# Kernel tuning notes

Measured on AMD Instinct MI355X. Metric: run time of the kernel, lower is better.

Reference implementation:

```python
import jax, jax.numpy as jnp
import numpy as np

N = 500_000          # number of particles
D = 6                # phase-space dimension
N_BINS = 128         # bins per axis
SQRT2 = 1.4142135623730951
BANDWIDTH = 1.0      # kernel width relative to bin width (module default)


def setup_inputs() -> dict:
    key = jax.random.key(0)
    x = jax.random.normal(key, (N, D), dtype=jnp.float32)
    edges = jnp.linspace(-3.0, 3.0, N_BINS + 1, dtype=jnp.float32)
    return {"x": x, "bin_edges_x": edges, "bin_edges_y": edges}


def _cdf_weights(u, edges, bw):
    """Per-point Gaussian mass in each bin via CDF (erf) differences.

    u: (n,), edges: (m+1,) -> weights (n, m); row sums <= 1.
    """
    z = jax.scipy.special.erf((edges[None, :] - u[:, None]) / (bw * SQRT2))  # (n, m+1)
    return 0.5 * (z[:, 1:] - z[:, :-1])  # (n, m)


def reference(x, bin_edges_x, bin_edges_y):
    dx = bin_edges_x[1] - bin_edges_x[0]
    dy = bin_edges_y[1] - bin_edges_y[0]
    bw_x = BANDWIDTH * dx
    bw_y = BANDWIDTH * dy
    # axis = (0, 1): project onto first two phase-space coordinates
    wx = _cdf_weights(x[:, 0], bin_edges_x, bw_x)  # (n, bx)
    wy = _cdf_weights(x[:, 1], bin_edges_y, bw_y)  # (n, by)
    hist = jnp.einsum('ni,nj->ij', wx, wy)         # (bx, by)
    # normalize to a probability density over the grid
    hist = hist / (hist.sum() * dx * dy)
    return hist
```

## Files before the change

### kernel.cpp

```cpp
#include <hip/hip_runtime.h>
#include <math.h>


#define NBINS   128
#define NB2     (NBINS * NBINS)
#define LDH     129
#define THREADS 1024
#define NBLOCKS 256
#define QSCALE  320.0f

static __device__ __forceinline__ unsigned short f2bf(float f) {
    unsigned int b = __float_as_uint(f);
    b += 0x7fff + ((b >> 16) & 1);
    return (unsigned short)(b >> 16);
}
static __device__ __forceinline__ float bf2f(unsigned short u) {
    return __uint_as_float((unsigned int)u << 16);
}

static __device__ __forceinline__ float erf_fast(float x) {
    const float ax = fabsf(x);
    const float t  = __builtin_amdgcn_rcpf(fmaf(0.3275911f, ax, 1.0f));
    const float e  = __expf(-x * x);
    float p = fmaf(1.061405429f, t, -1.453152027f);
    p = fmaf(p, t, 1.421413741f);
    p = fmaf(p, t, -0.284496736f);
    p = fmaf(p, t, 0.254829592f);
    p = p * t;
    return copysignf(fmaf(-p, e, 1.0f), x);
}

static __device__ __forceinline__ void axis_q(
    float u, float e0, float inv, int& b0, int q[8])
{
    const float cc = 0.7071067811865476f;
    const float spos = (u - e0) * inv;
    int b = (int)floorf(spos + 0.5f) - 4;
    b0 = b < 0 ? 0 : (b > NBINS - 8 ? NBINS - 8 : b);
    const float t0 = ((float)b0 - spos) * cc;
    float z[9];
    #pragma unroll
    for (int k = 0; k < 9; ++k) z[k] = erf_fast(t0 + (float)k * cc);
    #pragma unroll
    for (int k = 0; k < 8; ++k)
        q[k] = (int)rintf(0.5f * (z[k + 1] - z[k]) * QSCALE);
}

__global__ __launch_bounds__(THREADS, 4) void hist_sparse_kernel(
    const float* __restrict__ x,
    const float* __restrict__ edges_x,
    const float* __restrict__ edges_y,
    unsigned short* __restrict__ partials,
    float* __restrict__ btot,
    int n)
{
    __shared__ int lh[NBINS * LDH];
    __shared__ int xw[16];

    const int tid  = threadIdx.x;
    const int lane = tid & 63;
    const int wv   = tid >> 6;

    for (int i = tid; i < NBINS * LDH; i += THREADS) lh[i] = 0;

    const float e0x = edges_x[0];
    const float dxw = edges_x[1] - e0x;
    const float e0y = edges_y[0];
    const float dyw = edges_y[1] - e0y;
    const float ivx = 1.0f / dxw;
    const float ivy = 1.0f / dyw;
    __syncthreads();

    int bsum = 0;
    const int stride = gridDim.x * THREADS;
    for (int p = blockIdx.x * THREADS + tid; p < n; p += stride) {
        const float2 u = *(const float2*)(x + (size_t)p * 6);
        int bx0, by0, qx[8], qy[8];
        axis_q(u.x, e0x, ivx, bx0, qx);
        axis_q(u.y, e0y, ivy, by0, qy);

        int sx = 0, sy = 0;
        #pragma unroll
        for (int k = 0; k < 8; ++k) { sx += qx[k]; sy += qy[k]; }
        bsum += sx * sy;

        int* const base = lh + bx0 * LDH + by0;
        #pragma unroll
        for (int i = 0; i < 8; ++i) {
            const int qi = qx[i];
            #pragma unroll
            for (int j = 0; j < 8; ++j)
                atomicAdd(base + i * LDH + j, qi * qy[j]);
        }
    }
    __syncthreads();

    {
        const float qs = 1.0f / (QSCALE * QSCALE);
        unsigned short* my = partials + (size_t)blockIdx.x * NB2;
        #pragma unroll
        for (int v = 0; v < 4; ++v) {
            const int e = tid * 16 + v * 4;
            const int r = e >> 7;
            const int c = e & 127;
            const int* row = lh + r * LDH + c;
            ushort4 o;
            o.x = f2bf((float)row[0] * qs);
            o.y = f2bf((float)row[1] * qs);
            o.z = f2bf((float)row[2] * qs);
            o.w = f2bf((float)row[3] * qs);
            *(ushort4*)(my + e) = o;
        }
    }

    #pragma unroll
    for (int off = 32; off > 0; off >>= 1) bsum += __shfl_down(bsum, off, 64);
    if (lane == 0) xw[wv] = bsum;
    __syncthreads();
    if (tid == 0) {
        const float qs = 1.0f / (QSCALE * QSCALE);
        int s = 0;
        #pragma unroll
        for (int k = 0; k < 16; ++k) s += xw[k];
        btot[blockIdx.x] = (float)s * qs;
    }
}

__global__ void reduce_kernel(const unsigned short* __restrict__ partials,
                              const float* __restrict__ btot,
                              const float* __restrict__ edges_x,
                              const float* __restrict__ edges_y,
                              float* __restrict__ out)
{
    __shared__ float4 red[16][16];
    __shared__ float ws[4];
    __shared__ float stot;

    const int t = threadIdx.x;
    const int bin4 = t & 15;
    const int pg = t >> 4;
    const int binBase = blockIdx.x * 64;

    float tl = btot[t];
    #pragma unroll
    for (int off = 32; off > 0; off >>= 1) tl += __shfl_down(tl, off, 64);
    if ((t & 63) == 0) ws[t >> 6] = tl;

    const unsigned short* p =
        partials + (size_t)(pg * 16) * NB2 + binBase + bin4 * 4;
    float4 s = {0.f, 0.f, 0.f, 0.f};
    #pragma unroll 8
    for (int k = 0; k < 16; ++k) {
        const ushort4 v = *(const ushort4*)(p + (size_t)k * NB2);
        s.x += bf2f(v.x); s.y += bf2f(v.y); s.z += bf2f(v.z); s.w += bf2f(v.w);
    }
    red[pg][bin4] = s;
    __syncthreads();

    if (t == 0) {
        const float dxw = edges_x[1] - edges_x[0];
        const float dyw = edges_y[1] - edges_y[0];
        stot = 1.0f / ((ws[0] + ws[1] + ws[2] + ws[3]) * dxw * dyw);
    }
    __syncthreads();

    if (t < 16) {
        float4 a = red[0][t];
        #pragma unroll
        for (int g = 1; g < 16; ++g) {
            const float4 b = red[g][t];
            a.x += b.x; a.y += b.y; a.z += b.z; a.w += b.w;
        }
        a.x *= stot; a.y *= stot; a.z *= stot; a.w *= stot;
        *(float4*)(out + binBase + t * 4) = a;
    }
}

extern "C" void kernel_launch(void* const* d_in, const int* in_sizes, int n_in,
                              void* d_out, int out_size, void* d_ws, size_t ws_size,
                              hipStream_t stream)
{
    const float* x  = (const float*)d_in[0];
    const float* ex = (const float*)d_in[1];
    const float* ey = (const float*)d_in[2];
    float* out = (float*)d_out;
    const int n = in_sizes[0] / 6;

    unsigned short* partials = (unsigned short*)d_ws;
    float* btot = (float*)((char*)d_ws + (size_t)NBLOCKS * NB2 * 2);

    hist_sparse_kernel<<<NBLOCKS, THREADS, 0, stream>>>(x, ex, ey, partials, btot, n);
    reduce_kernel<<<NB2 / 64, 256, 0, stream>>>(partials, btot, ex, ey, out);
}
```

Measured before the change: 76.39 us.

## Replace per-point erf evaluation with shared LUT and skip zero-weight atomics

Each block precomputes a 1024-entry shared-memory table of packed 8-bit quantized bin weights indexed by the fractional sub-bin offset. Per-particle erf evaluations become a table lookup plus byte unpacking. The 8-bin window is now centered on the particle instead of clamped at the edges, with explicit bounds checks. Atomic adds are skipped for zero products and wave-uniformly zero rows, which cuts LDS atomic traffic. The trade-off is quantization of the sub-bin position, which adds approximation error, plus extra branching.

```diff
diff --git a/kernel.cpp b/kernel.cpp
--- a/kernel.cpp
+++ b/kernel.cpp
@@ -30,22 +30,6 @@
     return copysignf(fmaf(-p, e, 1.0f), x);
 }
 
-static __device__ __forceinline__ void axis_q(
-    float u, float e0, float inv, int& b0, int q[8])
-{
-    const float cc = 0.7071067811865476f;
-    const float spos = (u - e0) * inv;
-    int b = (int)floorf(spos + 0.5f) - 4;
-    b0 = b < 0 ? 0 : (b > NBINS - 8 ? NBINS - 8 : b);
-    const float t0 = ((float)b0 - spos) * cc;
-    float z[9];
-    #pragma unroll
-    for (int k = 0; k < 9; ++k) z[k] = erf_fast(t0 + (float)k * cc);
-    #pragma unroll
-    for (int k = 0; k < 8; ++k)
-        q[k] = (int)rintf(0.5f * (z[k + 1] - z[k]) * QSCALE);
-}
-
 __global__ __launch_bounds__(THREADS, 4) void hist_sparse_kernel(
     const float* __restrict__ x,
     const float* __restrict__ edges_x,
@@ -55,12 +39,32 @@
     int n)
 {
     __shared__ int lh[NBINS * LDH];
+    __shared__ int2 lut[1024];
     __shared__ int xw[16];
 
     const int tid  = threadIdx.x;
     const int lane = tid & 63;
     const int wv   = tid >> 6;
 
+    {
+        const float cc = 0.7071067811865476f;
+        const float d = ((float)tid + 0.5f) * (1.0f / 1024.0f) - 0.5f;
+        float z[9];
+        #pragma unroll
+        for (int k = 0; k < 9; ++k)
+            z[k] = erf_fast(((float)k - 4.0f - d) * cc);
+        unsigned int lo = 0, hi = 0;
+        #pragma unroll
+        for (int k = 0; k < 4; ++k) {
+            const unsigned int qa =
+                (unsigned int)(int)rintf(0.5f * (z[k + 1] - z[k]) * QSCALE);
+            const unsigned int qb =
+                (unsigned int)(int)rintf(0.5f * (z[k + 5] - z[k + 4]) * QSCALE);
+            lo |= qa << (8 * k);
+            hi |= qb << (8 * k);
+        }
+        lut[tid] = make_int2((int)lo, (int)hi);
+    }
     for (int i = tid; i < NBINS * LDH; i += THREADS) lh[i] = 0;
 
     const float e0x = edges_x[0];
@@ -75,22 +79,52 @@
     const int stride = gridDim.x * THREADS;
     for (int p = blockIdx.x * THREADS + tid; p < n; p += stride) {
         const float2 u = *(const float2*)(x + (size_t)p * 6);
-        int bx0, by0, qx[8], qy[8];
-        axis_q(u.x, e0x, ivx, bx0, qx);
-        axis_q(u.y, e0y, ivy, by0, qy);
-
-        int sx = 0, sy = 0;
-        #pragma unroll
-        for (int k = 0; k < 8; ++k) { sx += qx[k]; sy += qy[k]; }
-        bsum += sx * sy;
-
-        int* const base = lh + bx0 * LDH + by0;
+
+        const float sposx = (u.x - e0x) * ivx;
+        const float rx = floorf(sposx + 0.5f);
+        const int b0x = (int)rx - 4;
+        int tix = (int)((sposx - rx + 0.5f) * 1024.0f);
+        tix = tix < 0 ? 0 : (tix > 1023 ? 1023 : tix);
+        const int2 wxp = lut[tix];
+
+        const float sposy = (u.y - e0y) * ivy;
+        const float ry = floorf(sposy + 0.5f);
+        const int b0y = (int)ry - 4;
+        int tiy = (int)((sposy - ry + 0.5f) * 1024.0f);
+        tiy = tiy < 0 ? 0 : (tiy > 1023 ? 1023 : tiy);
+        const int2 wyp = lut[tiy];
+
+        int qx[8], qy[8];
+        #pragma unroll
+        for (int k = 0; k < 4; ++k) {
+            qx[k]     = ((unsigned int)wxp.x >> (8 * k)) & 0xFF;
+            qx[k + 4] = ((unsigned int)wxp.y >> (8 * k)) & 0xFF;
+            qy[k]     = ((unsigned int)wyp.x >> (8 * k)) & 0xFF;
+            qy[k + 4] = ((unsigned int)wyp.y >> (8 * k)) & 0xFF;
+        }
+
+        int sxin = 0, syin = 0;
+        #pragma unroll
+        for (int k = 0; k < 8; ++k) {
+            if ((unsigned)(b0x + k) < (unsigned)NBINS) sxin += qx[k];
+            if ((unsigned)(b0y + k) < (unsigned)NBINS) syin += qy[k];
+        }
+        bsum += sxin * syin;
+
         #pragma unroll
         for (int i = 0; i < 8; ++i) {
             const int qi = qx[i];
-            #pragma unroll
-            for (int j = 0; j < 8; ++j)
-                atomicAdd(base + i * LDH + j, qi * qy[j]);
+            const int bx = b0x + i;
+            if (__any(qi != 0)) {
+                const bool vx = (unsigned)bx < (unsigned)NBINS;
+                int* const rowp = lh + bx * LDH + b0y;
+                #pragma unroll
+                for (int j = 0; j < 8; ++j) {
+                    const int prod = qi * qy[j];
+                    if (vx && (unsigned)(b0y + j) < (unsigned)NBINS && prod)
+                        atomicAdd(rowp + j, prod);
+                }
+            }
         }
     }
     __syncthreads();
```

Result: no change. 77.89 us (+2.0%).
